# Performance work log

Hardware: AMD Instinct MI355X
Metric: run time of the kernel (lower is better)

## Reference

```python
import jax, jax.numpy as jnp
import numpy as np

E = 8          # num_experts
K = 2          # num_experts_per_tok
NORM_TOPK = True
B, S, D, F = 2, 1024, 2048, 1024  # batch, seq, hidden, moe_intermediate


def _kaiming_uniform(key, shape):
    # moe_fused_kaiming_uniform_: bound = sqrt(3*5 / in_features), in_features = shape[-1]
    bound = float(np.sqrt(3.0 * 5.0 / shape[-1]))
    return jax.random.uniform(key, shape, jnp.float32, -bound, bound)


def setup_inputs() -> dict:
    key = jax.random.key(0)
    k0, k1, k2, k3, k4 = jax.random.split(key, 5)
    gate_bound = float(1.0 / np.sqrt(D))  # nn.Linear default init
    return {
        "hidden_states": jax.random.normal(k0, (B, S, D), jnp.float32),
        "gate_w": jax.random.uniform(k1, (E, D), jnp.float32, -gate_bound, gate_bound),
        "w_gate_proj": _kaiming_uniform(k2, (E, F, D)),
        "w_up_proj": _kaiming_uniform(k3, (E, F, D)),
        "w_down_proj": _kaiming_uniform(k4, (E, D, F)),
    }


def reference(hidden_states, gate_w, w_gate_proj, w_up_proj, w_down_proj):
    b, s, d = hidden_states.shape
    x = hidden_states.reshape(-1, d)                      # [T, D]
    T = x.shape[0]

    # Router: softmax in fp32, top-k, optional renorm
    router_logits = x @ gate_w.T                          # [T, E]
    probs = jax.nn.softmax(router_logits.astype(jnp.float32), axis=-1)
    routing_weights, selected = jax.lax.top_k(probs, K)   # [T, K], [T, K]
    if NORM_TOPK:
        routing_weights = routing_weights / routing_weights.sum(-1, keepdims=True)
    routing_weights = routing_weights.astype(x.dtype)

    # Dense combine weights: c[t, e] = sum_k rw[t,k] * (sel[t,k]==e)
    combine = jnp.zeros((T, E), x.dtype).at[jnp.arange(T)[:, None], selected].add(routing_weights)

    # Expert SwiGLU FFN (dense over experts; combine zeros out unrouted experts,
    # identical math to sorted grouped-GEMM dispatch in the original)
    g = jnp.einsum('td,efd->tef', x, w_gate_proj)         # [T, E, F]
    u = jnp.einsum('td,efd->tef', x, w_up_proj)           # [T, E, F]
    h = jax.nn.silu(g) * u                                # [T, E, F]
    out = jnp.einsum('tef,edf,te->td', h, w_down_proj, combine)  # [T, D]

    return out.reshape(b, s, d), router_logits
```

## Files before the change

### kernel.cpp

```cpp
#include <hip/hip_runtime.h>
#include <stdint.h>

#define T_TOK 2048
#define DIM   2048
#define FDIM  1024
#define NE    8
#define MAXTILES 40

typedef __attribute__((ext_vector_type(8))) short short8;
typedef __attribute__((ext_vector_type(4))) float f32x4;

__device__ __forceinline__ unsigned short f2b(float f) {
  union { float f; unsigned int i; } x; x.f = f;
  unsigned int r = x.i + 0x7fffu + ((x.i >> 16) & 1u);
  return (unsigned short)(r >> 16);
}

__device__ __forceinline__ void async16(void* lds, const void* g) {
  __builtin_amdgcn_global_load_lds(
      (const __attribute__((address_space(1))) void*)g,
      (__attribute__((address_space(3))) void*)lds, 16, 0, 0);
}

__global__ __launch_bounds__(256) void cvt_x_k(const float* __restrict__ x,
                                               unsigned short* __restrict__ xb)
{
  int i = (blockIdx.x * 256 + threadIdx.x) * 8;
  float4 a = *(const float4*)(x + i);
  float4 b = *(const float4*)(x + i + 4);
  ushort4 o0, o1;
  o0.x = f2b(a.x); o0.y = f2b(a.y); o0.z = f2b(a.z); o0.w = f2b(a.w);
  o1.x = f2b(b.x); o1.y = f2b(b.y); o1.z = f2b(b.z); o1.w = f2b(b.w);
  *(ushort4*)(xb + i) = o0;
  *(ushort4*)(xb + i + 4) = o1;
}

__global__ __launch_bounds__(256) void router_k(
    const float* __restrict__ x, const float* __restrict__ gw,
    float* __restrict__ topkw, int* __restrict__ topke, int* __restrict__ counts,
    float* __restrict__ logits_out)
{
  int wave = threadIdx.x >> 6, lane = threadIdx.x & 63;
  int t = blockIdx.x * 4 + wave;
  const float* xr = x + (size_t)t * DIM;
  float acc[NE];
#pragma unroll
  for (int e = 0; e < NE; e++) acc[e] = 0.f;
  for (int d = lane * 4; d < DIM; d += 256) {
    float4 xv = *(const float4*)(xr + d);
#pragma unroll
    for (int e = 0; e < NE; e++) {
      float4 gv = *(const float4*)(gw + e * DIM + d);
      acc[e] += xv.x * gv.x + xv.y * gv.y + xv.z * gv.z + xv.w * gv.w;
    }
  }
#pragma unroll
  for (int off = 32; off > 0; off >>= 1) {
#pragma unroll
    for (int e = 0; e < NE; e++) acc[e] += __shfl_down(acc[e], off);
  }
  if (lane == 0) {
    float m = acc[0];
#pragma unroll
    for (int e = 1; e < NE; e++) m = fmaxf(m, acc[e]);
    float p[NE];
#pragma unroll
    for (int e = 0; e < NE; e++) p[e] = __expf(acc[e] - m);
    int e0 = 0;
#pragma unroll
    for (int e = 1; e < NE; e++) if (acc[e] > acc[e0]) e0 = e;
    int e1 = -1;
#pragma unroll
    for (int e = 0; e < NE; e++) if (e != e0 && (e1 < 0 || acc[e] > acc[e1])) e1 = e;
    float s = p[e0] + p[e1];
    topkw[t * 2] = p[e0] / s;
    topkw[t * 2 + 1] = p[e1] / s;
    topke[t * 2] = e0; topke[t * 2 + 1] = e1;
    atomicAdd(&counts[e0], 1);
    atomicAdd(&counts[e1], 1);
#pragma unroll
    for (int e = 0; e < NE; e++) logits_out[t * NE + e] = acc[e];
  }
}

__global__ void scan_k(const int* __restrict__ counts, int* __restrict__ offsets,
                       int* __restrict__ cursors, int4* __restrict__ tiles,
                       int* __restrict__ ntiles)
{
  if (threadIdx.x == 0 && blockIdx.x == 0) {
    int o = 0, nt = 0;
    for (int e = 0; e < NE; e++) {
      offsets[e] = o; cursors[e] = o;
      int c = counts[e];
      for (int r = 0; r < c; r += 128) {
        int rows = c - r < 128 ? c - r : 128;
        tiles[nt] = make_int4(e, o + r, rows, 0);
        nt++;
      }
      o += c;
    }
    offsets[NE] = o;
    *ntiles = nt;
  }
}

__global__ void scatter_k(const int* __restrict__ topke, int* __restrict__ cursors,
                          int* __restrict__ perm)
{
  int i = blockIdx.x * blockDim.x + threadIdx.x;
  int e = topke[i];
  int s = atomicAdd(&cursors[e], 1);
  perm[s] = i;
}

__global__ __launch_bounds__(256) void gemm1_k(
    const unsigned short* __restrict__ xb,
    const float* __restrict__ wg,
    const float* __restrict__ wu,
    const int* __restrict__ perm, const float* __restrict__ topkw,
    const int4* __restrict__ tiles, const int* __restrict__ ntiles,
    unsigned short* __restrict__ H)
{
  __shared__ short As[128 * 32];
  __shared__ short Bgs[64 * 32];
  __shared__ short Bus[64 * 32];
  __shared__ int rowtok[128];
  __shared__ float roww[128];

  if (blockIdx.x >= *ntiles) return;
  int4 tm = tiles[blockIdx.x];
  int e = tm.x, row0 = tm.y, nrows = tm.z;
  int tid = threadIdx.x;
  if (tid < 128) {
    int r = tid < nrows ? tid : (nrows - 1);
    int pid = perm[row0 + r];
    rowtok[tid] = pid >> 1;
    roww[tid] = topkw[pid];
  }
  __syncthreads();

  int f0 = blockIdx.y * 64;
  int crow = tid >> 2;
  int ccol = (tid & 3) * 8;
  const unsigned short* a0 = xb + (size_t)rowtok[crow] * DIM + ccol;
  const unsigned short* a1 = xb + (size_t)rowtok[crow + 64] * DIM + ccol;
  const float* bg32 = wg + ((size_t)e * FDIM + f0 + crow) * DIM + ccol;
  const float* bu32 = wu + ((size_t)e * FDIM + f0 + crow) * DIM + ccol;
  short* as0 = As + tid * 8;
  short* as1 = As + (256 + tid) * 8;

  int wave = tid >> 6, lane = tid & 63;
  int wm = wave >> 1, wn = wave & 1;
  int lrow = lane & 15, quad = lane >> 4;

  f32x4 accg[4][2], accu[4][2];
#pragma unroll
  for (int i = 0; i < 4; i++)
#pragma unroll
    for (int j = 0; j < 2; j++) {
      accg[i][j] = (f32x4){0.f, 0.f, 0.f, 0.f};
      accu[i][j] = (f32x4){0.f, 0.f, 0.f, 0.f};
    }

  const short* arp = As + (wm * 64 + lrow) * 32 + quad * 8;
  const short* bgp = Bgs + (wn * 32 + lrow) * 32 + quad * 8;
  const short* bup = Bus + (wn * 32 + lrow) * 32 + quad * 8;

#pragma unroll 1
  for (int k0 = 0; k0 < DIM; k0 += 32) {
    async16(as0, a0 + k0);
    async16(as1, a1 + k0);
    float4 g0 = *(const float4*)(bg32 + k0);
    float4 g1 = *(const float4*)(bg32 + k0 + 4);
    float4 u0 = *(const float4*)(bu32 + k0);
    float4 u1 = *(const float4*)(bu32 + k0 + 4);
    short8 gs, us;
    gs[0] = f2b(g0.x); gs[1] = f2b(g0.y); gs[2] = f2b(g0.z); gs[3] = f2b(g0.w);
    gs[4] = f2b(g1.x); gs[5] = f2b(g1.y); gs[6] = f2b(g1.z); gs[7] = f2b(g1.w);
    us[0] = f2b(u0.x); us[1] = f2b(u0.y); us[2] = f2b(u0.z); us[3] = f2b(u0.w);
    us[4] = f2b(u1.x); us[5] = f2b(u1.y); us[6] = f2b(u1.z); us[7] = f2b(u1.w);
    *(short8*)(Bgs + tid * 8) = gs;
    *(short8*)(Bus + tid * 8) = us;
    __syncthreads();
    short8 af[4], bgf[2], buf2[2];
#pragma unroll
    for (int i = 0; i < 4; i++) af[i] = *(const short8*)(arp + i * 16 * 32);
#pragma unroll
    for (int j = 0; j < 2; j++) {
      bgf[j]  = *(const short8*)(bgp + j * 16 * 32);
      buf2[j] = *(const short8*)(bup + j * 16 * 32);
    }
#pragma unroll
    for (int i = 0; i < 4; i++)
#pragma unroll
      for (int j = 0; j < 2; j++) {
        accg[i][j] = __builtin_amdgcn_mfma_f32_16x16x32_bf16(af[i], bgf[j], accg[i][j], 0, 0, 0);
        accu[i][j] = __builtin_amdgcn_mfma_f32_16x16x32_bf16(af[i], buf2[j], accu[i][j], 0, 0, 0);
      }
    __syncthreads();
  }

#pragma unroll
  for (int i = 0; i < 4; i++) {
#pragma unroll
    for (int reg = 0; reg < 4; reg++) {
      int r = wm * 64 + i * 16 + quad * 4 + reg;
      if (r < nrows) {
        float w = roww[r];
#pragma unroll
        for (int j = 0; j < 2; j++) {
          float g = accg[i][j][reg], u = accu[i][j][reg];
          float h = g * u * w / (1.f + __expf(-g));
          H[(size_t)(row0 + r) * FDIM + f0 + wn * 32 + j * 16 + lrow] = f2b(h);
        }
      }
    }
  }
}

__global__ __launch_bounds__(256) void gemm2_k(
    const unsigned short* __restrict__ H,
    const float* __restrict__ wd,
    const int* __restrict__ perm,
    const int4* __restrict__ tiles, const int* __restrict__ ntiles,
    float* __restrict__ out)
{
  __shared__ short Hs[128 * 32];
  __shared__ short Bs[64 * 32];
  __shared__ int rowtok[128];

  if (blockIdx.x >= *ntiles) return;
  int4 tm = tiles[blockIdx.x];
  int e = tm.x, row0 = tm.y, nrows = tm.z;
  int tid = threadIdx.x;
  if (tid < 128) {
    int r = tid < nrows ? tid : (nrows - 1);
    rowtok[tid] = perm[row0 + r] >> 1;
  }
  __syncthreads();

  int d0 = blockIdx.y * 64;
  int crow = tid >> 2, ccol = (tid & 3) * 8;
  const unsigned short* a0 = H + (size_t)(row0 + crow) * FDIM + ccol;
  const unsigned short* a1 = H + (size_t)(row0 + crow + 64) * FDIM + ccol;
  const float* b32 = wd + ((size_t)e * DIM + d0 + crow) * FDIM + ccol;
  short* hs0 = Hs + tid * 8;
  short* hs1 = Hs + (256 + tid) * 8;

  int wave = tid >> 6, lane = tid & 63;
  int wm = wave >> 1, wn = wave & 1;
  int lrow = lane & 15, quad = lane >> 4;

  f32x4 acc[4][2];
#pragma unroll
  for (int i = 0; i < 4; i++)
#pragma unroll
    for (int j = 0; j < 2; j++) acc[i][j] = (f32x4){0.f, 0.f, 0.f, 0.f};

  const short* arp = Hs + (wm * 64 + lrow) * 32 + quad * 8;
  const short* brp = Bs + (wn * 32 + lrow) * 32 + quad * 8;

#pragma unroll 1
  for (int k0 = 0; k0 < FDIM; k0 += 32) {
    async16(hs0, a0 + k0);
    async16(hs1, a1 + k0);
    float4 b0 = *(const float4*)(b32 + k0);
    float4 b1 = *(const float4*)(b32 + k0 + 4);
    short8 bsv;
    bsv[0] = f2b(b0.x); bsv[1] = f2b(b0.y); bsv[2] = f2b(b0.z); bsv[3] = f2b(b0.w);
    bsv[4] = f2b(b1.x); bsv[5] = f2b(b1.y); bsv[6] = f2b(b1.z); bsv[7] = f2b(b1.w);
    *(short8*)(Bs + tid * 8) = bsv;
    __syncthreads();
    short8 af[4], bf[2];
#pragma unroll
    for (int i = 0; i < 4; i++) af[i] = *(const short8*)(arp + i * 16 * 32);
#pragma unroll
    for (int j = 0; j < 2; j++) bf[j] = *(const short8*)(brp + j * 16 * 32);
#pragma unroll
    for (int i = 0; i < 4; i++)
#pragma unroll
      for (int j = 0; j < 2; j++)
        acc[i][j] = __builtin_amdgcn_mfma_f32_16x16x32_bf16(af[i], bf[j], acc[i][j], 0, 0, 0);
    __syncthreads();
  }

#pragma unroll
  for (int i = 0; i < 4; i++) {
#pragma unroll
    for (int reg = 0; reg < 4; reg++) {
      int r = wm * 64 + i * 16 + quad * 4 + reg;
      if (r < nrows) {
        int t = rowtok[r];
#pragma unroll
        for (int j = 0; j < 2; j++) {
          atomicAdd(&out[(size_t)t * DIM + d0 + wn * 32 + j * 16 + lrow], acc[i][j][reg]);
        }
      }
    }
  }
}

extern "C" void kernel_launch(void* const* d_in, const int* in_sizes, int n_in,
                              void* d_out, int out_size, void* d_ws, size_t ws_size,
                              hipStream_t stream)
{
  const float* x  = (const float*)d_in[0];
  const float* gw = (const float*)d_in[1];
  const float* wg = (const float*)d_in[2];
  const float* wu = (const float*)d_in[3];
  const float* wd = (const float*)d_in[4];
  float* out = (float*)d_out;
  float* logits_out = out + (size_t)T_TOK * DIM;

  char* ws = (char*)d_ws;
  float* topkw   = (float*)(ws + 0);
  int*   topke   = (int*)(ws + 16384);
  int*   counts  = (int*)(ws + 32768);
  int*   offsets = (int*)(ws + 32768 + 64);
  int*   cursors = (int*)(ws + 32768 + 128);
  int*   ntiles  = (int*)(ws + 32768 + 192);
  int4*  tiles   = (int4*)(ws + 32768 + 256);
  int*   perm    = (int*)(ws + 32768 + 2048);
  unsigned short* xb = (unsigned short*)(ws + (1 << 16));
  unsigned short* H  = (unsigned short*)(ws + (12u << 20));

  hipMemsetAsync(d_out, 0, (size_t)out_size * sizeof(float), stream);
  hipMemsetAsync(counts, 0, 64, stream);

  cvt_x_k<<<(T_TOK * DIM) / 2048, 256, 0, stream>>>(x, xb);
  router_k<<<T_TOK / 4, 256, 0, stream>>>(x, gw, topkw, topke, counts, logits_out);
  scan_k<<<1, 64, 0, stream>>>(counts, offsets, cursors, tiles, ntiles);
  scatter_k<<<(T_TOK * 2) / 256, 256, 0, stream>>>(topke, cursors, perm);
  gemm1_k<<<dim3(MAXTILES, FDIM / 64), 256, 0, stream>>>(xb, wg, wu, perm, topkw, tiles, ntiles, H);
  gemm2_k<<<dim3(MAXTILES, DIM / 64), 256, 0, stream>>>(H, wd, perm, tiles, ntiles, out);
}
```

Before: 432.3 us.

## Pre-convert expert weights to bf16 and double GEMM K-tile to 64

Adds separate conversion passes that turn the gate, up and down expert weights into bf16 copies in workspace when it is large enough. The GEMM kernels then stream those bf16 copies straight into LDS with async loads, replacing per-block fp32 loads and in-loop conversion. The K step also doubles from 32 to 64 so each barrier pair covers twice as many MFMAs. The cost is converting every expert's weights on each call, which adds weight traffic, plus a larger LDS footprint per block.

```diff
diff --git a/kernel.cpp b/kernel.cpp
--- a/kernel.cpp
+++ b/kernel.cpp
@@ -22,17 +22,17 @@
       (__attribute__((address_space(3))) void*)lds, 16, 0, 0);
 }
 
-__global__ __launch_bounds__(256) void cvt_x_k(const float* __restrict__ x,
-                                               unsigned short* __restrict__ xb)
-{
-  int i = (blockIdx.x * 256 + threadIdx.x) * 8;
-  float4 a = *(const float4*)(x + i);
-  float4 b = *(const float4*)(x + i + 4);
+__global__ __launch_bounds__(256) void cvt_k(const float* __restrict__ in,
+                                             unsigned short* __restrict__ out)
+{
+  size_t i = ((size_t)blockIdx.x * 256 + threadIdx.x) * 8;
+  float4 a = *(const float4*)(in + i);
+  float4 b = *(const float4*)(in + i + 4);
   ushort4 o0, o1;
   o0.x = f2b(a.x); o0.y = f2b(a.y); o0.z = f2b(a.z); o0.w = f2b(a.w);
   o1.x = f2b(b.x); o1.y = f2b(b.y); o1.z = f2b(b.z); o1.w = f2b(b.w);
-  *(ushort4*)(xb + i) = o0;
-  *(ushort4*)(xb + i + 4) = o1;
+  *(ushort4*)(out + i) = o0;
+  *(ushort4*)(out + i + 4) = o1;
 }
 
 __global__ __launch_bounds__(256) void router_k(
@@ -113,17 +113,20 @@
   perm[s] = i;
 }
 
+template <bool CVT>
 __global__ __launch_bounds__(256) void gemm1_k(
     const unsigned short* __restrict__ xb,
-    const float* __restrict__ wg,
-    const float* __restrict__ wu,
+    const unsigned short* __restrict__ wgb,
+    const unsigned short* __restrict__ wub,
+    const float* __restrict__ wg32,
+    const float* __restrict__ wu32,
     const int* __restrict__ perm, const float* __restrict__ topkw,
     const int4* __restrict__ tiles, const int* __restrict__ ntiles,
     unsigned short* __restrict__ H)
 {
-  __shared__ short As[128 * 32];
-  __shared__ short Bgs[64 * 32];
-  __shared__ short Bus[64 * 32];
+  __shared__ short As[128 * 64];
+  __shared__ short Bgs[64 * 64];
+  __shared__ short Bus[64 * 64];
   __shared__ int rowtok[128];
   __shared__ float roww[128];
 
@@ -140,14 +143,27 @@
   __syncthreads();
 
   int f0 = blockIdx.y * 64;
-  int crow = tid >> 2;
-  int ccol = (tid & 3) * 8;
-  const unsigned short* a0 = xb + (size_t)rowtok[crow] * DIM + ccol;
-  const unsigned short* a1 = xb + (size_t)rowtok[crow + 64] * DIM + ccol;
-  const float* bg32 = wg + ((size_t)e * FDIM + f0 + crow) * DIM + ccol;
-  const float* bu32 = wu + ((size_t)e * FDIM + f0 + crow) * DIM + ccol;
-  short* as0 = As + tid * 8;
-  short* as1 = As + (256 + tid) * 8;
+  int sub = tid & 7;
+  int srow = tid >> 3;
+
+  const unsigned short* ag[4];
+#pragma unroll
+  for (int c = 0; c < 4; c++)
+    ag[c] = xb + (size_t)rowtok[c * 32 + srow] * DIM + sub * 8;
+
+  const unsigned short *bg[2], *bu[2];
+  const float *bg32[2], *bu32[2];
+#pragma unroll
+  for (int c = 0; c < 2; c++) {
+    size_t row = (size_t)e * FDIM + f0 + c * 32 + srow;
+    if (CVT) {
+      bg[c] = wgb + row * DIM + sub * 8;
+      bu[c] = wub + row * DIM + sub * 8;
+    } else {
+      bg32[c] = wg32 + row * DIM + sub * 8;
+      bu32[c] = wu32 + row * DIM + sub * 8;
+    }
+  }
 
   int wave = tid >> 6, lane = tid & 63;
   int wm = wave >> 1, wn = wave & 1;
@@ -162,41 +178,55 @@
       accu[i][j] = (f32x4){0.f, 0.f, 0.f, 0.f};
     }
 
-  const short* arp = As + (wm * 64 + lrow) * 32 + quad * 8;
-  const short* bgp = Bgs + (wn * 32 + lrow) * 32 + quad * 8;
-  const short* bup = Bus + (wn * 32 + lrow) * 32 + quad * 8;
+  const short* arp = As + (wm * 64 + lrow) * 64 + quad * 8;
+  const short* bgp = Bgs + (wn * 32 + lrow) * 64 + quad * 8;
+  const short* bup = Bus + (wn * 32 + lrow) * 64 + quad * 8;
 
 #pragma unroll 1
-  for (int k0 = 0; k0 < DIM; k0 += 32) {
-    async16(as0, a0 + k0);
-    async16(as1, a1 + k0);
-    float4 g0 = *(const float4*)(bg32 + k0);
-    float4 g1 = *(const float4*)(bg32 + k0 + 4);
-    float4 u0 = *(const float4*)(bu32 + k0);
-    float4 u1 = *(const float4*)(bu32 + k0 + 4);
-    short8 gs, us;
-    gs[0] = f2b(g0.x); gs[1] = f2b(g0.y); gs[2] = f2b(g0.z); gs[3] = f2b(g0.w);
-    gs[4] = f2b(g1.x); gs[5] = f2b(g1.y); gs[6] = f2b(g1.z); gs[7] = f2b(g1.w);
-    us[0] = f2b(u0.x); us[1] = f2b(u0.y); us[2] = f2b(u0.z); us[3] = f2b(u0.w);
-    us[4] = f2b(u1.x); us[5] = f2b(u1.y); us[6] = f2b(u1.z); us[7] = f2b(u1.w);
-    *(short8*)(Bgs + tid * 8) = gs;
-    *(short8*)(Bus + tid * 8) = us;
+  for (int k0 = 0; k0 < DIM; k0 += 64) {
+#pragma unroll
+    for (int c = 0; c < 4; c++) async16(As + c * 2048 + tid * 8, ag[c] + k0);
+    if (CVT) {
+#pragma unroll
+      for (int c = 0; c < 2; c++) {
+        async16(Bgs + c * 2048 + tid * 8, bg[c] + k0);
+        async16(Bus + c * 2048 + tid * 8, bu[c] + k0);
+      }
+    } else {
+#pragma unroll
+      for (int c = 0; c < 2; c++) {
+        float4 g0 = *(const float4*)(bg32[c] + k0);
+        float4 g1 = *(const float4*)(bg32[c] + k0 + 4);
+        float4 u0 = *(const float4*)(bu32[c] + k0);
+        float4 u1 = *(const float4*)(bu32[c] + k0 + 4);
+        short8 gs, us;
+        gs[0] = f2b(g0.x); gs[1] = f2b(g0.y); gs[2] = f2b(g0.z); gs[3] = f2b(g0.w);
+        gs[4] = f2b(g1.x); gs[5] = f2b(g1.y); gs[6] = f2b(g1.z); gs[7] = f2b(g1.w);
+        us[0] = f2b(u0.x); us[1] = f2b(u0.y); us[2] = f2b(u0.z); us[3] = f2b(u0.w);
+        us[4] = f2b(u1.x); us[5] = f2b(u1.y); us[6] = f2b(u1.z); us[7] = f2b(u1.w);
+        *(short8*)(Bgs + c * 2048 + tid * 8) = gs;
+        *(short8*)(Bus + c * 2048 + tid * 8) = us;
+      }
+    }
     __syncthreads();
-    short8 af[4], bgf[2], buf2[2];
-#pragma unroll
-    for (int i = 0; i < 4; i++) af[i] = *(const short8*)(arp + i * 16 * 32);
-#pragma unroll
-    for (int j = 0; j < 2; j++) {
-      bgf[j]  = *(const short8*)(bgp + j * 16 * 32);
-      buf2[j] = *(const short8*)(bup + j * 16 * 32);
-    }
-#pragma unroll
-    for (int i = 0; i < 4; i++)
+#pragma unroll
+    for (int s = 0; s < 2; s++) {
+      short8 af[4], bgf[2], buf2[2];
+#pragma unroll
+      for (int i = 0; i < 4; i++) af[i] = *(const short8*)(arp + i * 16 * 64 + s * 32);
 #pragma unroll
       for (int j = 0; j < 2; j++) {
-        accg[i][j] = __builtin_amdgcn_mfma_f32_16x16x32_bf16(af[i], bgf[j], accg[i][j], 0, 0, 0);
-        accu[i][j] = __builtin_amdgcn_mfma_f32_16x16x32_bf16(af[i], buf2[j], accu[i][j], 0, 0, 0);
-      }
+        bgf[j]  = *(const short8*)(bgp + j * 16 * 64 + s * 32);
+        buf2[j] = *(const short8*)(bup + j * 16 * 64 + s * 32);
+      }
+#pragma unroll
+      for (int i = 0; i < 4; i++)
+#pragma unroll
+        for (int j = 0; j < 2; j++) {
+          accg[i][j] = __builtin_amdgcn_mfma_f32_16x16x32_bf16(af[i], bgf[j], accg[i][j], 0, 0, 0);
+          accu[i][j] = __builtin_amdgcn_mfma_f32_16x16x32_bf16(af[i], buf2[j], accu[i][j], 0, 0, 0);
+        }
+    }
     __syncthreads();
   }
 
@@ -218,15 +248,17 @@
   }
 }
 
+template <bool CVT>
 __global__ __launch_bounds__(256) void gemm2_k(
     const unsigned short* __restrict__ H,
-    const float* __restrict__ wd,
+    const unsigned short* __restrict__ wdb,
+    const float* __restrict__ wd32,
     const int* __restrict__ perm,
     const int4* __restrict__ tiles, const int* __restrict__ ntiles,
     float* __restrict__ out)
 {
-  __shared__ short Hs[128 * 32];
-  __shared__ short Bs[64 * 32];
+  __shared__ short Hs[128 * 64];
+  __shared__ short Bs[64 * 64];
   __shared__ int rowtok[128];
 
   if (blockIdx.x >= *ntiles) return;
@@ -240,12 +272,21 @@
   __syncthreads();
 
   int d0 = blockIdx.y * 64;
-  int crow = tid >> 2, ccol = (tid & 3) * 8;
-  const unsigned short* a0 = H + (size_t)(row0 + crow) * FDIM + ccol;
-  const unsigned short* a1 = H + (size_t)(row0 + crow + 64) * FDIM + ccol;
-  const float* b32 = wd + ((size_t)e * DIM + d0 + crow) * FDIM + ccol;
-  short* hs0 = Hs + tid * 8;
-  short* hs1 = Hs + (256 + tid) * 8;
+  int sub = tid & 7, srow = tid >> 3;
+
+  const unsigned short* ah[4];
+#pragma unroll
+  for (int c = 0; c < 4; c++)
+    ah[c] = H + (size_t)(row0 + c * 32 + srow) * FDIM + sub * 8;
+
+  const unsigned short* bw[2];
+  const float* bw32[2];
+#pragma unroll
+  for (int c = 0; c < 2; c++) {
+    size_t row = (size_t)e * DIM + d0 + c * 32 + srow;
+    if (CVT) bw[c] = wdb + row * FDIM + sub * 8;
+    else     bw32[c] = wd32 + row * FDIM + sub * 8;
+  }
 
   int wave = tid >> 6, lane = tid & 63;
   int wm = wave >> 1, wn = wave & 1;
@@ -257,30 +298,41 @@
 #pragma unroll
     for (int j = 0; j < 2; j++) acc[i][j] = (f32x4){0.f, 0.f, 0.f, 0.f};
 
-  const short* arp = Hs + (wm * 64 + lrow) * 32 + quad * 8;
-  const short* brp = Bs + (wn * 32 + lrow) * 32 + quad * 8;
+  const short* arp = Hs + (wm * 64 + lrow) * 64 + quad * 8;
+  const short* brp = Bs + (wn * 32 + lrow) * 64 + quad * 8;
 
 #pragma unroll 1
-  for (int k0 = 0; k0 < FDIM; k0 += 32) {
-    async16(hs0, a0 + k0);
-    async16(hs1, a1 + k0);
-    float4 b0 = *(const float4*)(b32 + k0);
-    float4 b1 = *(const float4*)(b32 + k0 + 4);
-    short8 bsv;
-    bsv[0] = f2b(b0.x); bsv[1] = f2b(b0.y); bsv[2] = f2b(b0.z); bsv[3] = f2b(b0.w);
-    bsv[4] = f2b(b1.x); bsv[5] = f2b(b1.y); bsv[6] = f2b(b1.z); bsv[7] = f2b(b1.w);
-    *(short8*)(Bs + tid * 8) = bsv;
+  for (int k0 = 0; k0 < FDIM; k0 += 64) {
+#pragma unroll
+    for (int c = 0; c < 4; c++) async16(Hs + c * 2048 + tid * 8, ah[c] + k0);
+    if (CVT) {
+#pragma unroll
+      for (int c = 0; c < 2; c++) async16(Bs + c * 2048 + tid * 8, bw[c] + k0);
+    } else {
+#pragma unroll
+      for (int c = 0; c < 2; c++) {
+        float4 b0 = *(const float4*)(bw32[c] + k0);
+        float4 b1 = *(const float4*)(bw32[c] + k0 + 4);
+        short8 bsv;
+        bsv[0] = f2b(b0.x); bsv[1] = f2b(b0.y); bsv[2] = f2b(b0.z); bsv[3] = f2b(b0.w);
+        bsv[4] = f2b(b1.x); bsv[5] = f2b(b1.y); bsv[6] = f2b(b1.z); bsv[7] = f2b(b1.w);
+        *(short8*)(Bs + c * 2048 + tid * 8) = bsv;
+      }
+    }
     __syncthreads();
-    short8 af[4], bf[2];
-#pragma unroll
-    for (int i = 0; i < 4; i++) af[i] = *(const short8*)(arp + i * 16 * 32);
-#pragma unroll
-    for (int j = 0; j < 2; j++) bf[j] = *(const short8*)(brp + j * 16 * 32);
-#pragma unroll
-    for (int i = 0; i < 4; i++)
-#pragma unroll
-      for (int j = 0; j < 2; j++)
-        acc[i][j] = __builtin_amdgcn_mfma_f32_16x16x32_bf16(af[i], bf[j], acc[i][j], 0, 0, 0);
+#pragma unroll
+    for (int s = 0; s < 2; s++) {
+      short8 af[4], bf[2];
+#pragma unroll
+      for (int i = 0; i < 4; i++) af[i] = *(const short8*)(arp + i * 16 * 64 + s * 32);
+#pragma unroll
+      for (int j = 0; j < 2; j++) bf[j] = *(const short8*)(brp + j * 16 * 64 + s * 32);
+#pragma unroll
+      for (int i = 0; i < 4; i++)
+#pragma unroll
+        for (int j = 0; j < 2; j++)
+          acc[i][j] = __builtin_amdgcn_mfma_f32_16x16x32_bf16(af[i], bf[j], acc[i][j], 0, 0, 0);
+    }
     __syncthreads();
   }
 
@@ -292,9 +344,8 @@
       if (r < nrows) {
         int t = rowtok[r];
 #pragma unroll
-        for (int j = 0; j < 2; j++) {
+        for (int j = 0; j < 2; j++)
           atomicAdd(&out[(size_t)t * DIM + d0 + wn * 32 + j * 16 + lrow], acc[i][j][reg]);
-        }
       }
     }
   }
@@ -316,21 +367,45 @@
   float* topkw   = (float*)(ws + 0);
   int*   topke   = (int*)(ws + 16384);
   int*   counts  = (int*)(ws + 32768);
-  int*   offsets = (int*)(ws + 32768 + 64);
-  int*   cursors = (int*)(ws + 32768 + 128);
-  int*   ntiles  = (int*)(ws + 32768 + 192);
-  int4*  tiles   = (int4*)(ws + 32768 + 256);
-  int*   perm    = (int*)(ws + 32768 + 2048);
-  unsigned short* xb = (unsigned short*)(ws + (1 << 16));
-  unsigned short* H  = (unsigned short*)(ws + (12u << 20));
+  int*   offsets = (int*)(ws + 32832);
+  int*   cursors = (int*)(ws + 32896);
+  int*   ntiles  = (int*)(ws + 32960);
+  int4*  tiles   = (int4*)(ws + 33024);
+  int*   perm    = (int*)(ws + 36864);
+  unsigned short* xb  = (unsigned short*)(ws + 65536);
+  unsigned short* H   = (unsigned short*)(ws + 8454144);
+  unsigned short* wgb = (unsigned short*)(ws + 17104896);
+  unsigned short* wub = (unsigned short*)(ws + 50659328);
+  unsigned short* wdb = (unsigned short*)(ws + 84213760);
+  const bool cvt1 = ws_size >= (size_t)84213760;
+  const bool cvt2 = ws_size >= (size_t)117768192;
 
   hipMemsetAsync(d_out, 0, (size_t)out_size * sizeof(float), stream);
   hipMemsetAsync(counts, 0, 64, stream);
 
-  cvt_x_k<<<(T_TOK * DIM) / 2048, 256, 0, stream>>>(x, xb);
+  cvt_k<<<(T_TOK * DIM) / 2048, 256, 0, stream>>>(x, xb);
+  if (cvt1) {
+    cvt_k<<<(NE * FDIM * DIM) / 2048, 256, 0, stream>>>(wg, wgb);
+    cvt_k<<<(NE * FDIM * DIM) / 2048, 256, 0, stream>>>(wu, wub);
+  }
+  if (cvt2) {
+    cvt_k<<<(NE * DIM * FDIM) / 2048, 256, 0, stream>>>(wd, wdb);
+  }
   router_k<<<T_TOK / 4, 256, 0, stream>>>(x, gw, topkw, topke, counts, logits_out);
   scan_k<<<1, 64, 0, stream>>>(counts, offsets, cursors, tiles, ntiles);
   scatter_k<<<(T_TOK * 2) / 256, 256, 0, stream>>>(topke, cursors, perm);
-  gemm1_k<<<dim3(MAXTILES, FDIM / 64), 256, 0, stream>>>(xb, wg, wu, perm, topkw, tiles, ntiles, H);
-  gemm2_k<<<dim3(MAXTILES, DIM / 64), 256, 0, stream>>>(H, wd, perm, tiles, ntiles, out);
-}
+  if (cvt1) {
+    gemm1_k<true><<<dim3(MAXTILES, FDIM / 64), 256, 0, stream>>>(
+        xb, wgb, wub, nullptr, nullptr, perm, topkw, tiles, ntiles, H);
+  } else {
+    gemm1_k<false><<<dim3(MAXTILES, FDIM / 64), 256, 0, stream>>>(
+        xb, nullptr, nullptr, wg, wu, perm, topkw, tiles, ntiles, H);
+  }
+  if (cvt2) {
+    gemm2_k<true><<<dim3(MAXTILES, DIM / 64), 256, 0, stream>>>(
+        H, wdb, nullptr, perm, tiles, ntiles, out);
+  } else {
+    gemm2_k<false><<<dim3(MAXTILES, DIM / 64), 256, 0, stream>>>(
+        H, nullptr, wd, perm, tiles, ntiles, out);
+  }
+}
```

Result: slower. 466.4 us (+7.9%).
